# Kernel tuning notes

Measured on AMD Instinct MI355X. Metric: run time of the kernel, lower is better.

Reference implementation:

```python
import jax, jax.numpy as jnp
import numpy as np
import math

N_HEADS = 12
EPS = 1e-5

def _layernorm(x, w, b):
    # torch .var() is unbiased (ddof=1)
    mean = jnp.mean(x, axis=-1, keepdims=True)
    var = jnp.var(x, axis=-1, keepdims=True, ddof=1)
    return (x - mean) / jnp.sqrt(var + EPS) * w + b

def _gelu_tanh(x):
    c = math.sqrt(2.0 / math.pi)
    return 0.5 * x * (1.0 + jnp.tanh(c * (x + 0.044715 * x * x * x)))

def setup_inputs() -> dict:
    key = jax.random.key(0)
    ks = jax.random.split(key, 6)
    B, T, C = 4, 2048, 768
    s = 0.02
    return {
        "x": jax.random.normal(ks[0], (B, T, C), jnp.float32),
        "ln1_w": jnp.ones((C,), jnp.float32),
        "ln1_b": jnp.zeros((C,), jnp.float32),
        "c_attn_w": jax.random.normal(ks[1], (C, 3 * C), jnp.float32) * s,
        "c_attn_b": jnp.zeros((3 * C,), jnp.float32),
        "c_proj_w": jax.random.normal(ks[2], (C, C), jnp.float32) * s,
        "c_proj_b": jnp.zeros((C,), jnp.float32),
        "ln2_w": jnp.ones((C,), jnp.float32),
        "ln2_b": jnp.zeros((C,), jnp.float32),
        "fc_w": jax.random.normal(ks[3], (C, 4 * C), jnp.float32) * s,
        "fc_b": jnp.zeros((4 * C,), jnp.float32),
        "mproj_w": jax.random.normal(ks[4], (4 * C, C), jnp.float32) * s,
        "mproj_b": jnp.zeros((C,), jnp.float32),
    }

def _attention(x, c_attn_w, c_attn_b, c_proj_w, c_proj_b):
    B, T, C = x.shape
    H = N_HEADS
    D = C // H
    qkv = x @ c_attn_w + c_attn_b  # [B,T,3C]
    q, k, v = jnp.split(qkv, 3, axis=-1)
    q = q.reshape(B, T, H, D).transpose(0, 2, 1, 3)  # [B,H,T,D]
    k = k.reshape(B, T, H, D).transpose(0, 2, 1, 3)
    v = v.reshape(B, T, H, D).transpose(0, 2, 1, 3)
    scores = jnp.einsum("bhqd,bhkd->bhqk", q, k) * (D ** -0.5)  # [B,H,T,T]
    causal = jnp.tril(jnp.ones((T, T), bool))
    scores = jnp.where(causal[None, None], scores, jnp.float32(-jnp.inf))
    attn = jax.nn.softmax(scores, axis=-1)
    out = jnp.einsum("bhqk,bhkd->bhqd", attn, v)  # [B,H,T,D]
    out = out.transpose(0, 2, 1, 3).reshape(B, T, C)
    return out @ c_proj_w + c_proj_b

def reference(x, ln1_w, ln1_b, c_attn_w, c_attn_b, c_proj_w, c_proj_b,
              ln2_w, ln2_b, fc_w, fc_b, mproj_w, mproj_b):
    x = x + _attention(_layernorm(x, ln1_w, ln1_b), c_attn_w, c_attn_b, c_proj_w, c_proj_b)
    h = _gelu_tanh(_layernorm(x, ln2_w, ln2_b) @ fc_w + fc_b)
    return x + h @ mproj_w + mproj_b
```

## Files before the change

### kernel.cpp

```cpp
#include <hip/hip_runtime.h>
#include <hip/hip_bf16.h>
#include <cstdint>

#define BF __hip_bfloat16

typedef __bf16 v8bf __attribute__((ext_vector_type(8)));
typedef float  v4f  __attribute__((ext_vector_type(4)));

__device__ __forceinline__ float tof(BF v) { return __bfloat162float(v); }
__device__ __forceinline__ BF    tob(float v) { return __float2bfloat16(v); }
__device__ __forceinline__ float ldf(float v) { return v; }
__device__ __forceinline__ float ldf(BF v) { return tof(v); }
__device__ __forceinline__ void stv(float* p, float v) { *p = v; }
__device__ __forceinline__ void stv(BF* p, float v) { *p = tob(v); }

__device__ __forceinline__ v4f mfma16(v8bf a, v8bf b, v4f c) {
  return __builtin_amdgcn_mfma_f32_16x16x32_bf16(a, b, c, 0, 0, 0);
}

__device__ __forceinline__ void async16(const BF* g, BF* l) {
  __builtin_amdgcn_global_load_lds((const __attribute__((address_space(1))) void*)g,
                                   (__attribute__((address_space(3))) void*)l, 16, 0, 0);
}

__global__ __launch_bounds__(256) void transpose_k(const float* __restrict__ in,
                                                   BF* __restrict__ out, int R, int C) {
  __shared__ BF t[64][65];
  int tid = threadIdx.x;
  int c0 = blockIdx.x * 64, r0 = blockIdx.y * 64;
#pragma unroll
  for (int i = 0; i < 16; ++i) {
    int idx = i * 256 + tid;
    int rr = idx >> 6, cc = idx & 63;
    t[rr][cc] = tob(in[(size_t)(r0 + rr) * C + c0 + cc]);
  }
  __syncthreads();
#pragma unroll
  for (int i = 0; i < 16; ++i) {
    int idx = i * 256 + tid;
    int rr = idx >> 6, cc = idx & 63;
    out[(size_t)(c0 + rr) * R + r0 + cc] = t[cc][rr];
  }
}

__global__ __launch_bounds__(256) void prep_k(
    const float* __restrict__ caw, BF* __restrict__ oca,
    const float* __restrict__ pw,  BF* __restrict__ opj,
    const float* __restrict__ fw,  BF* __restrict__ ofc,
    const float* __restrict__ mw,  BF* __restrict__ omp,
    const float* __restrict__ x, const float* __restrict__ lw,
    const float* __restrict__ lb, BF* __restrict__ y) {
  __shared__ BF t[64][65];
  __shared__ float rs[4][2];
  const int bid = blockIdx.x;
  const int tid = threadIdx.x;
  if (bid < 1728) {
    const float* in; BF* out; int R, C, bx, by;
    if (bid < 432)       { in = caw; out = oca; R = 768;  C = 2304; bx = bid % 36; by = bid / 36; }
    else if (bid < 576)  { int i = bid - 432;  in = pw; out = opj; R = 768;  C = 768;  bx = i % 12; by = i / 12; }
    else if (bid < 1152) { int i = bid - 576;  in = fw; out = ofc; R = 768;  C = 3072; bx = i % 48; by = i / 48; }
    else                 { int i = bid - 1152; in = mw; out = omp; R = 3072; C = 768;  bx = i % 12; by = i / 12; }
    int c0 = bx * 64, r0 = by * 64;
#pragma unroll
    for (int i = 0; i < 16; ++i) {
      int idx = i * 256 + tid;
      int rr = idx >> 6, cc = idx & 63;
      t[rr][cc] = tob(in[(size_t)(r0 + rr) * C + c0 + cc]);
    }
    __syncthreads();
#pragma unroll
    for (int i = 0; i < 16; ++i) {
      int idx = i * 256 + tid;
      int rr = idx >> 6, cc = idx & 63;
      out[(size_t)(c0 + rr) * R + r0 + cc] = t[cc][rr];
    }
  } else {
    int row = bid - 1728;
    const float* xr = x + (size_t)row * 768;
    float v0 = xr[tid], v1 = xr[tid + 256], v2 = xr[tid + 512];
    float s1 = v0 + v1 + v2;
    float s2 = v0 * v0 + v1 * v1 + v2 * v2;
#pragma unroll
    for (int m = 32; m; m >>= 1) { s1 += __shfl_xor(s1, m); s2 += __shfl_xor(s2, m); }
    int wv = tid >> 6;
    if ((tid & 63) == 0) { rs[wv][0] = s1; rs[wv][1] = s2; }
    __syncthreads();
    s1 = rs[0][0] + rs[1][0] + rs[2][0] + rs[3][0];
    s2 = rs[0][1] + rs[1][1] + rs[2][1] + rs[3][1];
    float mean = s1 * (1.0f / 768.0f);
    float var = fmaxf((s2 - s1 * mean) * (1.0f / 767.0f), 0.0f);
    float rstd = rsqrtf(var + 1e-5f);
    BF* yr = y + (size_t)row * 768;
    yr[tid]       = tob((v0 - mean) * rstd * lw[tid]       + lb[tid]);
    yr[tid + 256] = tob((v1 - mean) * rstd * lw[tid + 256] + lb[tid + 256]);
    yr[tid + 512] = tob((v2 - mean) * rstd * lw[tid + 512] + lb[tid + 512]);
  }
}

__global__ __launch_bounds__(256) void vtrans_k(const BF* __restrict__ qkv,
                                                BF* __restrict__ vT) {
  __shared__ BF t[64][65];
  int tid = threadIdx.x;
  int t0 = blockIdx.x * 64;
  int bh = blockIdx.y;
  int b = bh / 12, h = bh % 12;
  const BF* src = qkv + (size_t)(b * 2048 + t0) * 2304 + 1536 + h * 64;
#pragma unroll
  for (int i = 0; i < 16; ++i) {
    int idx = i * 256 + tid;
    int rr = idx >> 6, cc = idx & 63;
    t[rr][cc] = src[(size_t)rr * 2304 + cc];
  }
  __syncthreads();
  BF* dst = vT + (size_t)bh * 64 * 2048 + t0;
#pragma unroll
  for (int i = 0; i < 16; ++i) {
    int idx = i * 256 + tid;
    int rr = idx >> 6, cc = idx & 63;
    dst[(size_t)rr * 2048 + cc] = t[cc][rr];
  }
}

template <typename TX>
__global__ __launch_bounds__(256) void ln_k(const TX* __restrict__ x,
                                            const float* __restrict__ w,
                                            const float* __restrict__ bia,
                                            BF* __restrict__ y) {
  int row = blockIdx.x, tid = threadIdx.x;
  const TX* xr = x + (size_t)row * 768;
  float v0 = ldf(xr[tid]), v1 = ldf(xr[tid + 256]), v2 = ldf(xr[tid + 512]);
  float s1 = v0 + v1 + v2;
  float s2 = v0 * v0 + v1 * v1 + v2 * v2;
#pragma unroll
  for (int m = 32; m; m >>= 1) { s1 += __shfl_xor(s1, m); s2 += __shfl_xor(s2, m); }
  __shared__ float rs[4][2];
  int wv = tid >> 6;
  if ((tid & 63) == 0) { rs[wv][0] = s1; rs[wv][1] = s2; }
  __syncthreads();
  s1 = rs[0][0] + rs[1][0] + rs[2][0] + rs[3][0];
  s2 = rs[0][1] + rs[1][1] + rs[2][1] + rs[3][1];
  float mean = s1 * (1.0f / 768.0f);
  float var = fmaxf((s2 - s1 * mean) * (1.0f / 767.0f), 0.0f);
  float rstd = rsqrtf(var + 1e-5f);
  BF* yr = y + (size_t)row * 768;
  yr[tid]       = tob((v0 - mean) * rstd * w[tid]       + bia[tid]);
  yr[tid + 256] = tob((v1 - mean) * rstd * w[tid + 256] + bia[tid + 256]);
  yr[tid + 512] = tob((v2 - mean) * rstd * w[tid + 512] + bia[tid + 512]);
}

__device__ __forceinline__ float gelu_f(float x) {
  float u = 0.7978845608028654f * (x + 0.044715f * x * x * x);
  float e = exp2f(2.8853900817779268f * u);
  return 0.5f * x * (1.0f + (1.0f - 2.0f / (e + 1.0f)));
}

template <int BN, int ACT, bool RESID, typename TR, typename TO>
__global__ __launch_bounds__(256) void gemm_sm_k(
    const BF* __restrict__ A, const BF* __restrict__ Bt, const float* __restrict__ bias,
    const TR* __restrict__ resid, TO* __restrict__ out, int M, int N, int K) {
  constexpr int NW = BN / 32;
  __shared__ __align__(16) BF As[2][128 * 64];
  __shared__ __align__(16) BF Bs[2][BN * 64];
  const int tid = threadIdx.x;
  const int w = tid >> 6, lane = tid & 63;
  const int quad = lane >> 4, l16 = lane & 15;
  const int gx = gridDim.x;
  const int nwg = gx * gridDim.y;
  const int lid = blockIdx.y * gx + blockIdx.x;
  const int swz = (lid & 7) * (nwg >> 3) + (lid >> 3);
  const int m0 = (swz / gx) * 128, n0 = (swz % gx) * BN;
  const int wm = (w >> 1) * 64, wn = (w & 1) * (BN / 2);
  const int sr = lane >> 3;
  const int sc = ((lane & 7) ^ sr) * 8;

  v4f acc[4][NW];
#pragma unroll
  for (int i = 0; i < 4; ++i)
#pragma unroll
    for (int j = 0; j < NW; ++j) acc[i][j] = (v4f){0.f, 0.f, 0.f, 0.f};

  auto stage = [&](int bsel, int k0) {
#pragma unroll
    for (int i = 0; i < 4; ++i) {
      int r0 = w * 32 + i * 8;
      async16(A + (size_t)(m0 + r0 + sr) * K + k0 + sc, &As[bsel][r0 * 64]);
    }
    if (BN == 128) {
#pragma unroll
      for (int i = 0; i < 4; ++i) {
        int r0 = w * 32 + i * 8;
        async16(Bt + (size_t)(n0 + r0 + sr) * K + k0 + sc, &Bs[bsel][r0 * 64]);
      }
    } else {
#pragma unroll
      for (int i = 0; i < 2; ++i) {
        int r0 = w * 16 + i * 8;
        async16(Bt + (size_t)(n0 + r0 + sr) * K + k0 + sc, &Bs[bsel][r0 * 64]);
      }
    }
  };

  const int nkt = K >> 6;
  stage(0, 0);
  __syncthreads();
  for (int kt = 0; kt < nkt; ++kt) {
    const int cur = kt & 1;
    if (kt + 1 < nkt) stage(cur ^ 1, (kt + 1) << 6);
#pragma unroll
    for (int kk = 0; kk < 2; ++kk) {
      v8bf af[4], bfv[NW];
#pragma unroll
      for (int mi = 0; mi < 4; ++mi) {
        int row = wm + mi * 16 + l16;
        af[mi] = *(const v8bf*)&As[cur][row * 64 + (((kk * 4 + quad) ^ (row & 7)) * 8)];
      }
#pragma unroll
      for (int nj = 0; nj < NW; ++nj) {
        int row = wn + nj * 16 + l16;
        bfv[nj] = *(const v8bf*)&Bs[cur][row * 64 + (((kk * 4 + quad) ^ (row & 7)) * 8)];
      }
      __builtin_amdgcn_s_setprio(1);
#pragma unroll
      for (int mi = 0; mi < 4; ++mi)
#pragma unroll
        for (int nj = 0; nj < NW; ++nj)
          acc[mi][nj] = mfma16(af[mi], bfv[nj], acc[mi][nj]);
      __builtin_amdgcn_s_setprio(0);
    }
    __syncthreads();
  }

#pragma unroll
  for (int nj = 0; nj < NW; ++nj) {
    int col = n0 + wn + nj * 16 + l16;
    float bv = bias[col];
#pragma unroll
    for (int mi = 0; mi < 4; ++mi) {
      v4f c = acc[mi][nj];
#pragma unroll
      for (int r = 0; r < 4; ++r) {
        int row = m0 + wm + mi * 16 + quad * 4 + r;
        float v = c[r] + bv;
        if (RESID) v += ldf(resid[(size_t)row * N + col]);
        if (ACT == 1) v = gelu_f(v);
        stv(&out[(size_t)row * N + col], v);
      }
    }
  }
}

template <int ACT, bool RESID, typename TR, typename TO>
__global__ __launch_bounds__(256) void gemm64_k(
    const BF* __restrict__ A, const BF* __restrict__ Bt, const float* __restrict__ bias,
    const TR* __restrict__ resid, TO* __restrict__ out, int M, int N, int K) {
  __shared__ __align__(16) BF As[2][64 * 64];
  __shared__ __align__(16) BF Bs[2][128 * 64];
  const int tid = threadIdx.x;
  const int w = tid >> 6, lane = tid & 63;
  const int quad = lane >> 4, l16 = lane & 15;
  const int gx = gridDim.x;
  const int nwg = gx * gridDim.y;
  const int lid = blockIdx.y * gx + blockIdx.x;
  const int swz = (lid & 7) * (nwg >> 3) + (lid >> 3);
  const int m0 = (swz / gx) * 64, n0 = (swz % gx) * 128;
  const int wm = (w >> 1) * 32, wn = (w & 1) * 64;
  const int sr = lane >> 3;
  const int sc = ((lane & 7) ^ sr) * 8;

  v4f acc[2][4];
#pragma unroll
  for (int i = 0; i < 2; ++i)
#pragma unroll
    for (int j = 0; j < 4; ++j) acc[i][j] = (v4f){0.f, 0.f, 0.f, 0.f};

  auto stage = [&](int bsel, int k0) {
#pragma unroll
    for (int i = 0; i < 2; ++i) {
      int r0 = w * 16 + i * 8;
      async16(A + (size_t)(m0 + r0 + sr) * K + k0 + sc, &As[bsel][r0 * 64]);
    }
#pragma unroll
    for (int i = 0; i < 4; ++i) {
      int r0 = w * 32 + i * 8;
      async16(Bt + (size_t)(n0 + r0 + sr) * K + k0 + sc, &Bs[bsel][r0 * 64]);
    }
  };

  const int nkt = K >> 6;
  stage(0, 0);
  __syncthreads();
  for (int kt = 0; kt < nkt; ++kt) {
    const int cur = kt & 1;
    if (kt + 1 < nkt) stage(cur ^ 1, (kt + 1) << 6);
#pragma unroll
    for (int kk = 0; kk < 2; ++kk) {
      v8bf af[2], bfv[4];
#pragma unroll
      for (int mi = 0; mi < 2; ++mi) {
        int row = wm + mi * 16 + l16;
        af[mi] = *(const v8bf*)&As[cur][row * 64 + (((kk * 4 + quad) ^ (row & 7)) * 8)];
      }
#pragma unroll
      for (int nj = 0; nj < 4; ++nj) {
        int row = wn + nj * 16 + l16;
        bfv[nj] = *(const v8bf*)&Bs[cur][row * 64 + (((kk * 4 + quad) ^ (row & 7)) * 8)];
      }
      __builtin_amdgcn_s_setprio(1);
#pragma unroll
      for (int mi = 0; mi < 2; ++mi)
#pragma unroll
        for (int nj = 0; nj < 4; ++nj)
          acc[mi][nj] = mfma16(af[mi], bfv[nj], acc[mi][nj]);
      __builtin_amdgcn_s_setprio(0);
    }
    __syncthreads();
  }

#pragma unroll
  for (int nj = 0; nj < 4; ++nj) {
    int col = n0 + wn + nj * 16 + l16;
    float bv = bias[col];
#pragma unroll
    for (int mi = 0; mi < 2; ++mi) {
      v4f c = acc[mi][nj];
#pragma unroll
      for (int r = 0; r < 4; ++r) {
        int row = m0 + wm + mi * 16 + quad * 4 + r;
        float v = c[r] + bv;
        if (RESID) v += ldf(resid[(size_t)row * N + col]);
        if (ACT == 1) v = gelu_f(v);
        stv(&out[(size_t)row * N + col], v);
      }
    }
  }
}

__global__ __launch_bounds__(256) void attn_k(const BF* __restrict__ qkv,
                                              const BF* __restrict__ vT,
                                              BF* __restrict__ out) {
  __shared__ __align__(16) BF Ks[64 * 64];
  __shared__ __align__(16) BF Vs[64 * 64];
  __shared__ __align__(16) BF Ps[4][16 * 64];
  const int tid = threadIdx.x;
  const int w = tid >> 6, lane = tid & 63;
  const int quad = lane >> 4, l16 = lane & 15;
  const int bid = blockIdx.x;
  const int qi = 31 - (bid / 48);
  const int bh = bid % 48;
  const int b = bh / 12, h = bh % 12;
  const int q0 = qi * 64;
  const int qf = q0 + w * 16;
  BF* Pw = &Ps[w][0];
  const float L2E = 1.4426950408889634f;

  auto sz = [](int r, int c) { return (r << 6) + (c ^ ((r & 7) << 3)); };

  const BF* qp = qkv + (size_t)(b * 2048 + qf + l16) * 2304 + h * 64;
  v8bf q0v = *(const v8bf*)(qp + quad * 8);
  v8bf q1v = *(const v8bf*)(qp + 32 + quad * 8);
#pragma unroll
  for (int i = 0; i < 8; ++i) {
    q0v[i] = (__bf16)(tof((BF)q0v[i]) * 0.125f);
    q1v[i] = (__bf16)(tof((BF)q1v[i]) * 0.125f);
  }
  v8bf ones;
#pragma unroll
  for (int i = 0; i < 8; ++i) ones[i] = (__bf16)1.0f;

  v4f O[4], S;
#pragma unroll
  for (int j = 0; j < 4; ++j) O[j] = (v4f){0.f, 0.f, 0.f, 0.f};
  S = (v4f){0.f, 0.f, 0.f, 0.f};

  const BF* kg = qkv + (size_t)b * 2048 * 2304 + 768 + h * 64;
  const BF* vg = vT + (size_t)bh * 64 * 2048;
  const int r0 = tid >> 3, c0 = (tid & 7) * 8;
  const int r1 = r0 + 32;
  const int nIter = qi + 1;

  v8bf nk0 = *(const v8bf*)(kg + (size_t)r0 * 2304 + c0);
  v8bf nk1 = *(const v8bf*)(kg + (size_t)r1 * 2304 + c0);
  v8bf nv0 = *(const v8bf*)(vg + (size_t)r0 * 2048 + c0);
  v8bf nv1 = *(const v8bf*)(vg + (size_t)r1 * 2048 + c0);

  for (int t = 0; t < nIter; ++t) {
    const int kt0 = t * 64;
    __syncthreads();
    *(v8bf*)&Ks[sz(r0, c0)] = nk0;
    *(v8bf*)&Ks[sz(r1, c0)] = nk1;
    *(v8bf*)&Vs[sz(r0, c0)] = nv0;
    *(v8bf*)&Vs[sz(r1, c0)] = nv1;
    __syncthreads();
    if (t + 1 < nIter) {
      const int kn = kt0 + 64;
      nk0 = *(const v8bf*)(kg + (size_t)(kn + r0) * 2304 + c0);
      nk1 = *(const v8bf*)(kg + (size_t)(kn + r1) * 2304 + c0);
      nv0 = *(const v8bf*)(vg + (size_t)r0 * 2048 + kn + c0);
      nv1 = *(const v8bf*)(vg + (size_t)r1 * 2048 + kn + c0);
    }
    v4f s[4];
    __builtin_amdgcn_s_setprio(1);
#pragma unroll
    for (int nt = 0; nt < 4; ++nt) {
      v8bf kf0 = *(const v8bf*)&Ks[sz(nt * 16 + l16, quad * 8)];
      v8bf kf1 = *(const v8bf*)&Ks[sz(nt * 16 + l16, 32 + quad * 8)];
      s[nt] = mfma16(q1v, kf1, mfma16(q0v, kf0, (v4f){0.f, 0.f, 0.f, 0.f}));
    }
    __builtin_amdgcn_s_setprio(0);
    if (t < qi) {
#pragma unroll
      for (int nt = 0; nt < 4; ++nt)
#pragma unroll
        for (int r = 0; r < 4; ++r)
          Pw[sz(quad * 4 + r, nt * 16 + l16)] = tob(exp2f(s[nt][r] * L2E));
    } else {
#pragma unroll
      for (int nt = 0; nt < 4; ++nt) {
        int key = kt0 + nt * 16 + l16;
#pragma unroll
        for (int r = 0; r < 4; ++r) {
          int qrow = qf + quad * 4 + r;
          float p = (key <= qrow) ? exp2f(s[nt][r] * L2E) : 0.f;
          Pw[sz(quad * 4 + r, nt * 16 + l16)] = tob(p);
        }
      }
    }
    asm volatile("s_waitcnt lgkmcnt(0)" ::: "memory");
    v8bf p0 = *(const v8bf*)&Pw[sz(l16, quad * 8)];
    v8bf p1 = *(const v8bf*)&Pw[sz(l16, 32 + quad * 8)];
    __builtin_amdgcn_s_setprio(1);
#pragma unroll
    for (int j = 0; j < 4; ++j) {
      v8bf vf0 = *(const v8bf*)&Vs[sz(j * 16 + l16, quad * 8)];
      v8bf vf1 = *(const v8bf*)&Vs[sz(j * 16 + l16, 32 + quad * 8)];
      O[j] = mfma16(p1, vf1, mfma16(p0, vf0, O[j]));
    }
    S = mfma16(p1, ones, mfma16(p0, ones, S));
    __builtin_amdgcn_s_setprio(0);
  }

#pragma unroll
  for (int r = 0; r < 4; ++r) {
    float inv = 1.0f / S[r];
    int row = b * 2048 + qf + quad * 4 + r;
    BF* op = out + (size_t)row * 768 + h * 64 + l16;
#pragma unroll
    for (int j = 0; j < 4; ++j) op[j * 16] = tob(O[j][r] * inv);
  }
}

extern "C" void kernel_launch(void* const* d_in, const int* in_sizes, int n_in,
                              void* d_out, int out_size, void* d_ws, size_t ws_size,
                              hipStream_t stream) {
  const float* x        = (const float*)d_in[0];
  const float* ln1_w    = (const float*)d_in[1];
  const float* ln1_b    = (const float*)d_in[2];
  const float* c_attn_w = (const float*)d_in[3];
  const float* c_attn_b = (const float*)d_in[4];
  const float* c_proj_w = (const float*)d_in[5];
  const float* c_proj_b = (const float*)d_in[6];
  const float* ln2_w    = (const float*)d_in[7];
  const float* ln2_b    = (const float*)d_in[8];
  const float* fc_w     = (const float*)d_in[9];
  const float* fc_b     = (const float*)d_in[10];
  const float* mproj_w  = (const float*)d_in[11];
  const float* mproj_b  = (const float*)d_in[12];
  float* out = (float*)d_out;
  char* wsb = (char*)d_ws;
  dim3 blk(256);

  BF* vT = (BF*)((char*)d_out + 12582912);

  const size_t NEED_BIG = 89653248;
  if (ws_size >= NEED_BIG) {
    BF* qkv      = (BF*)(wsb);
    BF* hbuf     = (BF*)(wsb);
    BF* x2       = (BF*)(wsb + 50331648);
    BF* wT_attn  = (BF*)(wsb + 62914560);
    BF* wT_proj  = (BF*)(wsb + 66453504);
    BF* wT_fc    = (BF*)(wsb + 67633152);
    BF* wT_mproj = (BF*)(wsb + 72351744);
    BF* lnbuf    = (BF*)(wsb + 77070336);
    BF* attnout  = (BF*)d_out;

    prep_k<<<dim3(9920), blk, 0, stream>>>(c_attn_w, wT_attn, c_proj_w, wT_proj,
                                           fc_w, wT_fc, mproj_w, wT_mproj,
                                           x, ln1_w, ln1_b, lnbuf);
    gemm_sm_k<128, 0, false, float, BF><<<dim3(18, 64), blk, 0, stream>>>(
        lnbuf, wT_attn, c_attn_b, (const float*)nullptr, qkv, 8192, 2304, 768);
    vtrans_k<<<dim3(32, 48), blk, 0, stream>>>(qkv, vT);
    attn_k<<<dim3(1536), blk, 0, stream>>>(qkv, vT, attnout);
    gemm_sm_k<64, 0, true, float, BF><<<dim3(12, 64), blk, 0, stream>>>(
        attnout, wT_proj, c_proj_b, x, x2, 8192, 768, 768);
    ln_k<BF><<<8192, blk, 0, stream>>>(x2, ln2_w, ln2_b, lnbuf);
    gemm64_k<1, false, float, BF><<<dim3(24, 128), blk, 0, stream>>>(
        lnbuf, wT_fc, fc_b, (const float*)nullptr, hbuf, 8192, 3072, 768);
    gemm_sm_k<64, 0, true, BF, float><<<dim3(12, 64), blk, 0, stream>>>(
        hbuf, wT_mproj, mproj_b, x2, out, 8192, 768, 3072);
  } else {
    BF* ws       = (BF*)d_ws;
    BF* qkv      = ws;
    BF* attnout  = ws + (size_t)18874368;
    BF* wT_attn  = attnout;
    BF* x2       = ws;
    BF* wT_proj  = ws + (size_t)6291456;
    BF* wT_fc    = ws + (size_t)6881280;
    BF* wT_mproj = ws + (size_t)9240576;
    BF* hbuf     = ws + (size_t)11599872;
    BF* lnbuf    = (BF*)d_out;

    transpose_k<<<dim3(36, 12), blk, 0, stream>>>(c_attn_w, wT_attn, 768, 2304);
    ln_k<float><<<8192, blk, 0, stream>>>(x, ln1_w, ln1_b, lnbuf);
    gemm_sm_k<128, 0, false, float, BF><<<dim3(18, 64), blk, 0, stream>>>(
        lnbuf, wT_attn, c_attn_b, (const float*)nullptr, qkv, 8192, 2304, 768);
    vtrans_k<<<dim3(32, 48), blk, 0, stream>>>(qkv, vT);
    attn_k<<<dim3(1536), blk, 0, stream>>>(qkv, vT, attnout);
    transpose_k<<<dim3(12, 12), blk, 0, stream>>>(c_proj_w, wT_proj, 768, 768);
    gemm_sm_k<64, 0, true, float, BF><<<dim3(12, 64), blk, 0, stream>>>(
        attnout, wT_proj, c_proj_b, x, x2, 8192, 768, 768);
    ln_k<BF><<<8192, blk, 0, stream>>>(x2, ln2_w, ln2_b, lnbuf);
    transpose_k<<<dim3(48, 12), blk, 0, stream>>>(fc_w, wT_fc, 768, 3072);
    transpose_k<<<dim3(12, 48), blk, 0, stream>>>(mproj_w, wT_mproj, 3072, 768);
    for (int half = 1; half >= 0; --half) {
      size_t r0 = (size_t)half * 4096;
      gemm_sm_k<128, 1, false, float, BF><<<dim3(24, 32), blk, 0, stream>>>(
          lnbuf + r0 * 768, wT_fc, fc_b, (const float*)nullptr, hbuf, 4096, 3072, 768);
      gemm_sm_k<64, 0, true, BF, float><<<dim3(12, 32), blk, 0, stream>>>(
          hbuf, wT_mproj, mproj_b, x2 + r0 * 768, out + r0 * 768, 4096, 768, 3072);
    }
  }
}
```

Baseline: 359.7 us.

## Replace FC GEMM with 256x256-tile 8-wave kernel using staggered async loads

Replaces the 64x128-tile FC GEMM with a 512-thread, 256x256-tile kernel in which each wave computes 128x64. The K loop is split into four sub-phases, with A halves and B tiles prefetched at different points using explicit vmcnt waits and raw barriers. The goal is higher arithmetic intensity per LDS load and better overlap of global loads with MFMA work. In exchange it uses 128 accumulator registers per lane and 128KB of LDS, so only one workgroup fits per CU and the grid drops to 384 blocks, which may underfill the device.

After: 381.1 us. +5.9%, slower.

```diff
diff --git a/kernel.cpp b/kernel.cpp
--- a/kernel.cpp
+++ b/kernel.cpp
@@ -249,85 +249,141 @@
   }
 }
 
-template <int ACT, bool RESID, typename TR, typename TO>
-__global__ __launch_bounds__(256) void gemm64_k(
-    const BF* __restrict__ A, const BF* __restrict__ Bt, const float* __restrict__ bias,
-    const TR* __restrict__ resid, TO* __restrict__ out, int M, int N, int K) {
-  __shared__ __align__(16) BF As[2][64 * 64];
-  __shared__ __align__(16) BF Bs[2][128 * 64];
+template <int ACT, typename TO>
+__global__ __launch_bounds__(512, 1) void gemm8_k(
+    const BF* __restrict__ A, const BF* __restrict__ Bt,
+    const float* __restrict__ bias, TO* __restrict__ out,
+    int M, int N, int K) {
+  __shared__ __align__(16) BF As[2][2][128 * 64];
+  __shared__ __align__(16) BF Bs[2][2][128 * 64];
   const int tid = threadIdx.x;
   const int w = tid >> 6, lane = tid & 63;
   const int quad = lane >> 4, l16 = lane & 15;
+  const int wr = w >> 2, wc = w & 3;
   const int gx = gridDim.x;
   const int nwg = gx * gridDim.y;
   const int lid = blockIdx.y * gx + blockIdx.x;
   const int swz = (lid & 7) * (nwg >> 3) + (lid >> 3);
-  const int m0 = (swz / gx) * 64, n0 = (swz % gx) * 128;
-  const int wm = (w >> 1) * 32, wn = (w & 1) * 64;
+  const int m0 = (swz / gx) * 256, n0 = (swz % gx) * 256;
   const int sr = lane >> 3;
   const int sc = ((lane & 7) ^ sr) * 8;
 
-  v4f acc[2][4];
-#pragma unroll
-  for (int i = 0; i < 2; ++i)
+  v4f acc[8][4];
+#pragma unroll
+  for (int i = 0; i < 8; ++i)
 #pragma unroll
     for (int j = 0; j < 4; ++j) acc[i][j] = (v4f){0.f, 0.f, 0.f, 0.f};
 
-  auto stage = [&](int bsel, int k0) {
-#pragma unroll
-    for (int i = 0; i < 2; ++i) {
-      int r0 = w * 16 + i * 8;
-      async16(A + (size_t)(m0 + r0 + sr) * K + k0 + sc, &As[bsel][r0 * 64]);
-    }
-#pragma unroll
-    for (int i = 0; i < 4; ++i) {
-      int r0 = w * 32 + i * 8;
-      async16(Bt + (size_t)(n0 + r0 + sr) * K + k0 + sc, &Bs[bsel][r0 * 64]);
-    }
+  auto stA = [&](int buf, int half, int kt) {
+    const int k0 = kt << 6;
+#pragma unroll
+    for (int r = 0; r < 2; ++r)
+      async16(A + (size_t)(m0 + half * 128 + r * 64 + w * 8 + sr) * K + k0 + sc,
+              &As[buf][half][(r * 64 + w * 8) * 64]);
   };
+  auto stB = [&](int buf, int half, int kt) {
+    const int k0 = kt << 6;
+#pragma unroll
+    for (int r = 0; r < 2; ++r)
+      async16(Bt + (size_t)(n0 + half * 128 + r * 64 + w * 8 + sr) * K + k0 + sc,
+              &Bs[buf][half][(r * 64 + w * 8) * 64]);
+  };
 
   const int nkt = K >> 6;
-  stage(0, 0);
-  __syncthreads();
+  stB(0, 0, 0); stB(0, 1, 0);
+  stA(0, 0, 0); stA(0, 1, 0);
+  stB(1, 0, 1); stB(1, 1, 1);
+
+  const int brow = (wc & 1) * 64;
   for (int kt = 0; kt < nkt; ++kt) {
-    const int cur = kt & 1;
-    if (kt + 1 < nkt) stage(cur ^ 1, (kt + 1) << 6);
-#pragma unroll
-    for (int kk = 0; kk < 2; ++kk) {
-      v8bf af[2], bfv[4];
-#pragma unroll
-      for (int mi = 0; mi < 2; ++mi) {
-        int row = wm + mi * 16 + l16;
-        af[mi] = *(const v8bf*)&As[cur][row * 64 + (((kk * 4 + quad) ^ (row & 7)) * 8)];
-      }
-#pragma unroll
-      for (int nj = 0; nj < 4; ++nj) {
-        int row = wn + nj * 16 + l16;
-        bfv[nj] = *(const v8bf*)&Bs[cur][row * 64 + (((kk * 4 + quad) ^ (row & 7)) * 8)];
-      }
-      __builtin_amdgcn_s_setprio(1);
-#pragma unroll
-      for (int mi = 0; mi < 2; ++mi)
-#pragma unroll
-        for (int nj = 0; nj < 4; ++nj)
-          acc[mi][nj] = mfma16(af[mi], bfv[nj], acc[mi][nj]);
-      __builtin_amdgcn_s_setprio(0);
-    }
-    __syncthreads();
+    const int buf = kt & 1;
+    const BF* Ah = &As[buf][wr][0];
+    const BF* Bh = &Bs[buf][wc >> 1][0];
+    v8bf a[4], b0[4], b1[4];
+    if (kt < nkt - 1) asm volatile("s_waitcnt vmcnt(4)" ::: "memory");
+    else              asm volatile("s_waitcnt vmcnt(0)" ::: "memory");
+    __builtin_amdgcn_s_barrier();
+    asm volatile("" ::: "memory");
+    if (kt + 1 < nkt) stA(buf ^ 1, 0, kt + 1);
+#pragma unroll
+    for (int nj = 0; nj < 4; ++nj) {
+      int r = brow + nj * 16 + l16;
+      b0[nj] = *(const v8bf*)&Bh[r * 64 + ((quad ^ (r & 7)) * 8)];
+    }
+#pragma unroll
+    for (int mi = 0; mi < 4; ++mi) {
+      int r = mi * 16 + l16;
+      a[mi] = *(const v8bf*)&Ah[r * 64 + ((quad ^ (r & 7)) * 8)];
+    }
+    __builtin_amdgcn_s_setprio(1);
+#pragma unroll
+    for (int mi = 0; mi < 4; ++mi)
+#pragma unroll
+      for (int nj = 0; nj < 4; ++nj)
+        acc[mi][nj] = mfma16(a[mi], b0[nj], acc[mi][nj]);
+    __builtin_amdgcn_s_setprio(0);
+    __builtin_amdgcn_s_barrier();
+    asm volatile("" ::: "memory");
+    if (kt + 1 < nkt) stA(buf ^ 1, 1, kt + 1);
+#pragma unroll
+    for (int mi = 0; mi < 4; ++mi) {
+      int r = (mi + 4) * 16 + l16;
+      a[mi] = *(const v8bf*)&Ah[r * 64 + ((quad ^ (r & 7)) * 8)];
+    }
+    __builtin_amdgcn_s_setprio(1);
+#pragma unroll
+    for (int mi = 0; mi < 4; ++mi)
+#pragma unroll
+      for (int nj = 0; nj < 4; ++nj)
+        acc[mi + 4][nj] = mfma16(a[mi], b0[nj], acc[mi + 4][nj]);
+    __builtin_amdgcn_s_setprio(0);
+    __builtin_amdgcn_s_barrier();
+    asm volatile("" ::: "memory");
+#pragma unroll
+    for (int nj = 0; nj < 4; ++nj) {
+      int r = brow + nj * 16 + l16;
+      b1[nj] = *(const v8bf*)&Bh[r * 64 + (((4 + quad) ^ (r & 7)) * 8)];
+    }
+#pragma unroll
+    for (int mi = 0; mi < 4; ++mi) {
+      int r = mi * 16 + l16;
+      a[mi] = *(const v8bf*)&Ah[r * 64 + (((4 + quad) ^ (r & 7)) * 8)];
+    }
+    __builtin_amdgcn_s_setprio(1);
+#pragma unroll
+    for (int mi = 0; mi < 4; ++mi)
+#pragma unroll
+      for (int nj = 0; nj < 4; ++nj)
+        acc[mi][nj] = mfma16(a[mi], b1[nj], acc[mi][nj]);
+    __builtin_amdgcn_s_setprio(0);
+    __builtin_amdgcn_s_barrier();
+    asm volatile("" ::: "memory");
+    if (kt + 2 < nkt) { stB(buf, 0, kt + 2); stB(buf, 1, kt + 2); }
+#pragma unroll
+    for (int mi = 0; mi < 4; ++mi) {
+      int r = (mi + 4) * 16 + l16;
+      a[mi] = *(const v8bf*)&Ah[r * 64 + (((4 + quad) ^ (r & 7)) * 8)];
+    }
+    __builtin_amdgcn_s_setprio(1);
+#pragma unroll
+    for (int mi = 0; mi < 4; ++mi)
+#pragma unroll
+      for (int nj = 0; nj < 4; ++nj)
+        acc[mi + 4][nj] = mfma16(a[mi], b1[nj], acc[mi + 4][nj]);
+    __builtin_amdgcn_s_setprio(0);
   }
 
 #pragma unroll
   for (int nj = 0; nj < 4; ++nj) {
-    int col = n0 + wn + nj * 16 + l16;
+    int col = n0 + wc * 64 + nj * 16 + l16;
     float bv = bias[col];
 #pragma unroll
-    for (int mi = 0; mi < 2; ++mi) {
+    for (int mi = 0; mi < 8; ++mi) {
       v4f c = acc[mi][nj];
 #pragma unroll
       for (int r = 0; r < 4; ++r) {
-        int row = m0 + wm + mi * 16 + quad * 4 + r;
+        int row = m0 + wr * 128 + mi * 16 + quad * 4 + r;
         float v = c[r] + bv;
-        if (RESID) v += ldf(resid[(size_t)row * N + col]);
         if (ACT == 1) v = gelu_f(v);
         stv(&out[(size_t)row * N + col], v);
       }
@@ -493,8 +549,8 @@
     gemm_sm_k<64, 0, true, float, BF><<<dim3(12, 64), blk, 0, stream>>>(
         attnout, wT_proj, c_proj_b, x, x2, 8192, 768, 768);
     ln_k<BF><<<8192, blk, 0, stream>>>(x2, ln2_w, ln2_b, lnbuf);
-    gemm64_k<1, false, float, BF><<<dim3(24, 128), blk, 0, stream>>>(
-        lnbuf, wT_fc, fc_b, (const float*)nullptr, hbuf, 8192, 3072, 768);
+    gemm8_k<1, BF><<<dim3(12, 32), dim3(512), 0, stream>>>(
+        lnbuf, wT_fc, fc_b, hbuf, 8192, 3072, 768);
     gemm_sm_k<64, 0, true, BF, float><<<dim3(12, 64), blk, 0, stream>>>(
         hbuf, wT_mproj, mproj_b, x2, out, 8192, 768, 3072);
   } else {
```
